# Kernel optimization log

Hardware: AMD Instinct MI355X
Metric: run time of the kernel (lower is better)

## Reference

```python
import jax, jax.numpy as jnp
import numpy as np

B, S, HID, QKV, H = 2, 4096, 1024, 1024, 16
HD = QKV // H  # head_dim = 64
KH, KW = 4, 1
SH, SW = 4, 1


def setup_inputs() -> dict:
    key = jax.random.key(0)
    ks = jax.random.split(key, 7)
    s = 1.0 / np.sqrt(HID)
    q = jax.random.normal(ks[0], (B, S, HID), dtype=jnp.float32)
    Wq = jax.random.uniform(ks[1], (HID, QKV), jnp.float32, -s, s)
    Wk = jax.random.uniform(ks[2], (HID, QKV), jnp.float32, -s, s)
    Wv = jax.random.uniform(ks[3], (HID, QKV), jnp.float32, -s, s)
    Wlin = jax.random.uniform(ks[4], (QKV, HID), jnp.float32, -1.0 / np.sqrt(QKV), 1.0 / np.sqrt(QKV))
    # depthwise conv weight: [out_ch=H, in_ch/groups=1, KH, KW]
    cs = 1.0 / np.sqrt(KH * KW)
    conv_w = jax.random.uniform(ks[5], (H, 1, KH, KW), jnp.float32, -cs, cs)
    log_temp = jnp.zeros((1,), dtype=jnp.float32)  # temperature='unit', frozen
    return {"q": q, "Wq": Wq, "Wk": Wk, "Wv": Wv, "Wlin": Wlin,
            "conv_w": conv_w, "log_temp": log_temp}


def split_heads(x):
    # [B, S, QKV] -> [B, H, S, HD]
    return x.reshape(B, -1, H, HD).transpose(0, 2, 1, 3)


def depthwise_conv(x, w):
    # x: [B, H, S, HD]; depthwise over channel dim H, window over (S, HD)
    return jax.lax.conv_general_dilated(
        x, w, window_strides=(SH, SW), padding='VALID',
        feature_group_count=H,
        dimension_numbers=('NCHW', 'OIHW', 'NCHW'))


def reference(q, Wq, Wk, Wv, Wlin, conv_w, log_temp):
    # self-attention path: k = v = q
    qh = split_heads(q @ Wq)          # [B,H,S,HD]
    kh = split_heads(q @ Wk)
    vh = split_heads(q @ Wv)
    qh = qh * (1.0 / jnp.exp(log_temp[0]))
    kc = depthwise_conv(kh, conv_w)   # [B,H,Sk,HD], Sk = (S-4)//4 + 1
    vc = depthwise_conv(vh, conv_w)
    logits_raw = jnp.einsum('bhqd,bhkd->bhqk', qh, kc)
    # shape changed after conv -> masks skipped (matches torch branch)
    att = jax.nn.softmax(logits_raw, axis=-1)
    out = jnp.einsum('bhqk,bhkd->bhqd', att, vc)  # [B,H,S,HD]
    out = out.transpose(0, 2, 1, 3).reshape(B, S, QKV)
    out = out @ Wlin                  # [B,S,HID]
    return (out, logits_raw)
```

## Files before the change

kernel.cpp:

```cpp
#include <hip/hip_runtime.h>
#include <hip/hip_bf16.h>
#include <stdint.h>


using short8 = __attribute__((ext_vector_type(8))) short;
using bf16x4 = __attribute__((ext_vector_type(4))) short;
using f32x4  = __attribute__((ext_vector_type(4))) float;

__device__ __forceinline__ float bf2f(short u) {
  union { float f; uint32_t i; } v; v.i = ((uint32_t)(uint16_t)u) << 16; return v.f;
}
__device__ __forceinline__ short f2bf(float f) {
  union { float f; uint32_t i; } v; v.f = f;
  uint32_t r = v.i + 0x7FFFu + ((v.i >> 16) & 1u);
  return (short)(uint16_t)(r >> 16);
}
__device__ __forceinline__ short f2bf_hw(float f) {
  __hip_bfloat16 h = __float2bfloat16(f);
  return *reinterpret_cast<short*>(&h);
}

__device__ __forceinline__ void async16(const void* g, void* l) {
  __builtin_amdgcn_global_load_lds(
      (const __attribute__((address_space(1))) void*)g,
      (__attribute__((address_space(3))) void*)l, 16, 0, 0);
}

__global__ void cvt8(const float* __restrict__ in, short* __restrict__ out) {
  const size_t i = ((size_t)blockIdx.x * 256 + threadIdx.x) * 8;
  float4 a = *(const float4*)(in + i);
  float4 b = *(const float4*)(in + i + 4);
  short8 o;
  o[0] = f2bf(a.x); o[1] = f2bf(a.y); o[2] = f2bf(a.z); o[3] = f2bf(a.w);
  o[4] = f2bf(b.x); o[5] = f2bf(b.y); o[6] = f2bf(b.z); o[7] = f2bf(b.w);
  *(short8*)(out + i) = o;
}

struct ConvT4Args { const float* s0; const float* s1; const float* s2;
                    const float* s3; short* out; };
__global__ void convT4(ConvT4Args a) {
  __shared__ float tile[64][65];
  const float* in = (blockIdx.z == 0) ? a.s0 : (blockIdx.z == 1) ? a.s1
                   : (blockIdx.z == 2) ? a.s2 : a.s3;
  short* out = a.out + (size_t)blockIdx.z * 1048576;
  const int c0 = blockIdx.x * 64, r0 = blockIdx.y * 64;
  const int tx = threadIdx.x & 63, ty = threadIdx.x >> 6;
  #pragma unroll
  for (int i = ty; i < 64; i += 4)
    tile[i][tx] = in[(size_t)(r0 + i) * 1024 + c0 + tx];
  __syncthreads();
  #pragma unroll
  for (int i = ty; i < 64; i += 4)
    out[(size_t)(c0 + i) * 1024 + r0 + tx] = f2bf(tile[tx][i]);
}

__global__ void transpose2d(const short* __restrict__ in, short* __restrict__ out,
                            int R, int C) {
  __shared__ short tile[64][65];
  const size_t zoff = (size_t)blockIdx.z * (size_t)R * (size_t)C;
  const int c0 = blockIdx.x * 64, r0 = blockIdx.y * 64;
  const int tx = threadIdx.x & 63, ty = threadIdx.x >> 6;
  #pragma unroll
  for (int i = ty; i < 64; i += 4)
    tile[i][tx] = in[zoff + (size_t)(r0 + i) * C + c0 + tx];
  __syncthreads();
  #pragma unroll
  for (int i = ty; i < 64; i += 4)
    out[zoff + (size_t)(c0 + i) * R + r0 + tx] = tile[tx][i];
}

struct GemmArgs {
  const short* A; const short* Bt;
  short* C; short* C2; short* C3; float* Cf;
  long sA, sB, sC;
  long zA, zB, zC;
  int  K;
  const float* ltemp;
  const float* cw;
  int  mode;
};

__global__ __launch_bounds__(256, 2)
void gemm_bt(GemmArgs g) {
  const int tid  = threadIdx.x;
  const int wave = tid >> 6, lane = tid & 63;
  const int l16 = lane & 15, l4 = lane >> 4;
  const int wm = wave & 1, wn = wave >> 1;
  const int m0 = blockIdx.y * 128, n0 = blockIdx.x * 128;
  const size_t zA = (size_t)blockIdx.z * g.zA;
  const size_t zB = (size_t)blockIdx.z * g.zB;
  const size_t zC = (size_t)blockIdx.z * g.zC;

  __shared__ __align__(16) short As[128 * 64];
  __shared__ __align__(16) short Bs[128 * 64];

  f32x4 acc[4][4] = {};

  const int srow = tid >> 3;
  const int scol = (tid & 7) << 3;
  const short* Abase = g.A + zA + (size_t)m0 * g.sA + scol;
  const short* Bbase = g.Bt + zB + (size_t)n0 * g.sB + scol;

  for (int k0 = 0; k0 < g.K; k0 += 64) {
    __syncthreads();
    #pragma unroll
    for (int c = 0; c < 4; ++c) {
      async16(Abase + (size_t)(c * 32 + srow) * g.sA + k0, &As[c * 2048 + wave * 512]);
      async16(Bbase + (size_t)(c * 32 + srow) * g.sB + k0, &Bs[c * 2048 + wave * 512]);
    }
    asm volatile("s_waitcnt vmcnt(0)" ::: "memory");
    __syncthreads();
    #pragma unroll
    for (int kk = 0; kk < 2; ++kk) {
      short8 a[4], b[4];
      #pragma unroll
      for (int t = 0; t < 4; ++t) {
        a[t] = *(const short8*)&As[(wm * 64 + t * 16 + l16) * 64 + kk * 32 + l4 * 8];
        b[t] = *(const short8*)&Bs[(wn * 64 + t * 16 + l16) * 64 + kk * 32 + l4 * 8];
      }
      #pragma unroll
      for (int i = 0; i < 4; ++i)
        #pragma unroll
        for (int j = 0; j < 4; ++j)
          acc[i][j] = __builtin_amdgcn_mfma_f32_16x16x32_bf16(a[i], b[j], acc[i][j], 0, 0, 0);
    }
  }

  if (g.mode == 0) {
    float* Cz = g.Cf + zC;
    #pragma unroll
    for (int i = 0; i < 4; ++i) {
      const int row = m0 + wm * 64 + i * 16 + l4 * 4;
      #pragma unroll
      for (int j = 0; j < 4; ++j) {
        const int col = n0 + wn * 64 + j * 16 + l16;
        #pragma unroll
        for (int rr = 0; rr < 4; ++rr)
          Cz[(size_t)(row + rr) * g.sC + col] = acc[i][j][rr];
      }
    }
  } else if (blockIdx.z == 0) {
    float sc = __expf(-g.ltemp[0]);
    short* Cz = g.C;
    #pragma unroll
    for (int i = 0; i < 4; ++i) {
      const int row = m0 + wm * 64 + i * 16 + l4 * 4;
      #pragma unroll
      for (int j = 0; j < 4; ++j) {
        const int col = n0 + wn * 64 + j * 16 + l16;
        const int hh = col >> 6, dd = col & 63;
        #pragma unroll
        for (int rr = 0; rr < 4; ++rr) {
          const int m = row + rr;
          const size_t off = (size_t)((m >> 12) * 16 + hh) * 262144
                           + (size_t)(m & 4095) * 64 + dd;
          Cz[off] = f2bf(acc[i][j][rr] * sc);
        }
      }
    }
  } else {
    const int h = (n0 + wn * 64) >> 6;
    float wv[4];
    #pragma unroll
    for (int t = 0; t < 4; ++t) wv[t] = g.cw[h * 4 + t];
    short* dst = (blockIdx.z == 1) ? g.C2 : g.C3;
    #pragma unroll
    for (int i = 0; i < 4; ++i) {
      const int row_base = m0 + wm * 64 + i * 16 + l4 * 4;
      const int b  = row_base >> 12;
      const int sk = (row_base & 4095) >> 2;
      #pragma unroll
      for (int j = 0; j < 4; ++j) {
        const int d = j * 16 + l16;
        float v = wv[0] * acc[i][j][0] + wv[1] * acc[i][j][1]
                + wv[2] * acc[i][j][2] + wv[3] * acc[i][j][3];
        dst[(size_t)(b * 16 + h) * 65536 + (size_t)sk * 64 + d] = f2bf(v);
      }
    }
  }
}

__global__ __launch_bounds__(256, 4)
void fused_attn(const short* __restrict__ qh, const short* __restrict__ kc,
                const short* __restrict__ vct,
                float* __restrict__ logits, short* __restrict__ oattn) {
  const int id = blockIdx.x;
  const int bh = id & 31;
  const int qt = id >> 5;
  const int tid = threadIdx.x;
  const int wave = tid >> 6, lane = tid & 63;
  const int l16 = lane & 15, l4 = lane >> 4;

  __shared__ __align__(16) short attb[4][32 * 128];
  short* const myatt = attb[wave];

  const int qg = qt * 128 + wave * 32;

  const short* qbase = qh + (size_t)bh * 262144 + (size_t)qg * 64;
  const short8 aQ0_0 = *(const short8*)(qbase + (size_t)l16 * 64 + l4 * 8);
  const short8 aQ0_1 = *(const short8*)(qbase + (size_t)l16 * 64 + 32 + l4 * 8);
  const short8 aQ1_0 = *(const short8*)(qbase + (size_t)(16 + l16) * 64 + l4 * 8);
  const short8 aQ1_1 = *(const short8*)(qbase + (size_t)(16 + l16) * 64 + 32 + l4 * 8);

  const short* kb = kc + (size_t)bh * 65536;
  const short* vb = vct + (size_t)bh * 65536;
  float* lgqA = logits + (size_t)bh * 4194304 + (size_t)(qg + l16) * 1024;
  float* lgqB = lgqA + 16 * 1024;

  const int sw = (l16 & 7) << 3;
  float psumA = 0.f, psumB = 0.f;
  f32x4 o0 = {}, o1 = {}, o2 = {}, o3 = {};
  f32x4 o4 = {}, o5 = {}, o6 = {}, o7 = {};

  for (int sec = 0; sec < 8; ++sec) {
    const int kbase = sec * 128;

    #pragma unroll 2
    for (int j = 0; j < 8; ++j) {
      const int kr = kbase + j * 16 + l16;
      short8 k0 = *(const short8*)(kb + (size_t)kr * 64 + l4 * 8);
      short8 k1 = *(const short8*)(kb + (size_t)kr * 64 + 32 + l4 * 8);
      f32x4 accA = {}, accB = {};
      accA = __builtin_amdgcn_mfma_f32_16x16x32_bf16(k0, aQ0_0, accA, 0, 0, 0);
      accA = __builtin_amdgcn_mfma_f32_16x16x32_bf16(k1, aQ0_1, accA, 0, 0, 0);
      accB = __builtin_amdgcn_mfma_f32_16x16x32_bf16(k0, aQ1_0, accB, 0, 0, 0);
      accB = __builtin_amdgcn_mfma_f32_16x16x32_bf16(k1, aQ1_1, accB, 0, 0, 0);

      *(f32x4*)(lgqA + kbase + j * 16 + l4 * 4) = accA;
      *(f32x4*)(lgqB + kbase + j * 16 + l4 * 4) = accB;

      bf16x4 pA, pB;
      #pragma unroll
      for (int rr = 0; rr < 4; ++rr) {
        const float eA = __expf(accA[rr]);
        const float eB = __expf(accB[rr]);
        psumA += eA;
        psumB += eB;
        pA[rr] = f2bf_hw(eA);
        pB[rr] = f2bf_hw(eB);
      }
      const int pc = (j * 16 + l4 * 4) ^ sw;
      *(bf16x4*)&myatt[l16 * 128 + pc] = pA;
      *(bf16x4*)&myatt[(16 + l16) * 128 + pc] = pB;
    }

    #pragma unroll
    for (int c = 0; c < 4; ++c) {
      const int cb = kbase + c * 32 + l4 * 8;
      const int cl = (c * 32 + l4 * 8) ^ sw;
      short8 paA = *(const short8*)&myatt[l16 * 128 + cl];
      short8 paB = *(const short8*)&myatt[(16 + l16) * 128 + cl];
      short8 v0 = *(const short8*)(vb + (size_t)(l16)      * 1024 + cb);
      short8 v1 = *(const short8*)(vb + (size_t)(16 + l16) * 1024 + cb);
      short8 v2 = *(const short8*)(vb + (size_t)(32 + l16) * 1024 + cb);
      short8 v3 = *(const short8*)(vb + (size_t)(48 + l16) * 1024 + cb);
      o0 = __builtin_amdgcn_mfma_f32_16x16x32_bf16(paA, v0, o0, 0, 0, 0);
      o1 = __builtin_amdgcn_mfma_f32_16x16x32_bf16(paA, v1, o1, 0, 0, 0);
      o2 = __builtin_amdgcn_mfma_f32_16x16x32_bf16(paA, v2, o2, 0, 0, 0);
      o3 = __builtin_amdgcn_mfma_f32_16x16x32_bf16(paA, v3, o3, 0, 0, 0);
      o4 = __builtin_amdgcn_mfma_f32_16x16x32_bf16(paB, v0, o4, 0, 0, 0);
      o5 = __builtin_amdgcn_mfma_f32_16x16x32_bf16(paB, v1, o5, 0, 0, 0);
      o6 = __builtin_amdgcn_mfma_f32_16x16x32_bf16(paB, v2, o6, 0, 0, 0);
      o7 = __builtin_amdgcn_mfma_f32_16x16x32_bf16(paB, v3, o7, 0, 0, 0);
    }
  }

  psumA += __shfl_xor(psumA, 16, 64);
  psumA += __shfl_xor(psumA, 32, 64);
  psumB += __shfl_xor(psumB, 16, 64);
  psumB += __shfl_xor(psumB, 32, 64);
  float invA[4], invB[4];
  #pragma unroll
  for (int rr = 0; rr < 4; ++rr) {
    invA[rr] = 1.0f / __shfl(psumA, l4 * 4 + rr, 64);
    invB[rr] = 1.0f / __shfl(psumB, l4 * 4 + rr, 64);
  }

  short* op = oattn + ((size_t)(bh >> 4) * 4096 + qg) * 1024 + (bh & 15) * 64;
  #pragma unroll
  for (int rr = 0; rr < 4; ++rr) {
    const size_t ra = (size_t)(l4 * 4 + rr) * 1024;
    op[ra + l16]      = f2bf(o0[rr] * invA[rr]);
    op[ra + 16 + l16] = f2bf(o1[rr] * invA[rr]);
    op[ra + 32 + l16] = f2bf(o2[rr] * invA[rr]);
    op[ra + 48 + l16] = f2bf(o3[rr] * invA[rr]);
    const size_t rb = (size_t)(16 + l4 * 4 + rr) * 1024;
    op[rb + l16]      = f2bf(o4[rr] * invB[rr]);
    op[rb + 16 + l16] = f2bf(o5[rr] * invB[rr]);
    op[rb + 32 + l16] = f2bf(o6[rr] * invB[rr]);
    op[rb + 48 + l16] = f2bf(o7[rr] * invB[rr]);
  }
}

extern "C" void kernel_launch(void* const* d_in, const int* in_sizes, int n_in,
                              void* d_out, int out_size, void* d_ws, size_t ws_size,
                              hipStream_t stream) {
  const float* q    = (const float*)d_in[0];
  const float* Wq   = (const float*)d_in[1];
  const float* Wk   = (const float*)d_in[2];
  const float* Wv   = (const float*)d_in[3];
  const float* Wlin = (const float*)d_in[4];
  const float* cw   = (const float*)d_in[5];
  const float* lt   = (const float*)d_in[6];

  float* out_f    = (float*)d_out;
  float* logits_f = out_f + 8388608;

  short* ws    = (short*)d_ws;
  short* Wt    = ws;
  short* Xb    = ws + 4194304;
  short* QKVq  = ws + 12582912;
  short* Kc    = ws + 20971520;
  short* Vc    = ws + 23068672;
  short* Vct   = ws + 25165824;
  short* oattn = Xb;

  cvt8<<<dim3(4096), 256, 0, stream>>>(q, Xb);

  ConvT4Args ca = { Wq, Wk, Wv, Wlin, Wt };
  convT4<<<dim3(16, 16, 4), 256, 0, stream>>>(ca);

  GemmArgs gq = {};
  gq.A = Xb; gq.Bt = Wt; gq.C = QKVq; gq.C2 = Kc; gq.C3 = Vc;
  gq.sA = 1024; gq.sB = 1024; gq.sC = 0;
  gq.zA = 0; gq.zB = 1048576; gq.zC = 0;
  gq.K = 1024; gq.ltemp = lt; gq.cw = cw; gq.mode = 3;
  gemm_bt<<<dim3(8, 64, 3), 256, 0, stream>>>(gq);

  transpose2d<<<dim3(1, 16, 32), 256, 0, stream>>>(Vc, Vct, 1024, 64);

  fused_attn<<<dim3(1024), 256, 0, stream>>>(QKVq, Kc, Vct, logits_f, oattn);

  GemmArgs gf = {};
  gf.A = oattn; gf.Bt = Wt + 3145728; gf.Cf = out_f;
  gf.sA = 1024; gf.sB = 1024; gf.sC = 1024;
  gf.zA = 0; gf.zB = 0; gf.zC = 0;
  gf.K = 1024; gf.mode = 0;
  gemm_bt<<<dim3(8, 64, 1), 256, 0, stream>>>(gf);
}
```

Measured before the change: 309.1 us.

## Stage K and V tiles in shared LDS with async double buffering

Each block now cooperatively loads 64-row K and V tiles into LDS with async global-to-LDS copies, double-buffered across 16 half-sections. The four waves then share those tiles instead of each issuing its own global loads for K and V. The per-wave probability buffer shrinks to match the smaller step. LDS use per block grows and the occupancy hint drops from 4 to 3 blocks. The change also adds a barrier per step and relies on a vmcnt wait count that must line up with the interleaved logits stores.

Measured after the change: 281.5 us. -8.9%, faster.

```diff
diff --git a/kernel.cpp b/kernel.cpp
--- a/kernel.cpp
+++ b/kernel.cpp
@@ -180,7 +180,7 @@
   }
 }
 
-__global__ __launch_bounds__(256, 4)
+__global__ __launch_bounds__(256, 3)
 void fused_attn(const short* __restrict__ qh, const short* __restrict__ kc,
                 const short* __restrict__ vct,
                 float* __restrict__ logits, short* __restrict__ oattn) {
@@ -191,7 +191,9 @@
   const int wave = tid >> 6, lane = tid & 63;
   const int l16 = lane & 15, l4 = lane >> 4;
 
-  __shared__ __align__(16) short attb[4][32 * 128];
+  __shared__ __align__(16) short Ks[2][4096];
+  __shared__ __align__(16) short Vs[2][4096];
+  __shared__ __align__(16) short attb[4][2048];
   short* const myatt = attb[wave];
 
   const int qg = qt * 128 + wave * 32;
@@ -207,19 +209,46 @@
   float* lgqA = logits + (size_t)bh * 4194304 + (size_t)(qg + l16) * 1024;
   float* lgqB = lgqA + 16 * 1024;
 
+  const int strow = tid >> 3;
+  const int schunk = (tid & 7) ^ (strow & 7);
+  const int sdst = tid * 8;
+
   const int sw = (l16 & 7) << 3;
   float psumA = 0.f, psumB = 0.f;
   f32x4 o0 = {}, o1 = {}, o2 = {}, o3 = {};
   f32x4 o4 = {}, o5 = {}, o6 = {}, o7 = {};
 
-  for (int sec = 0; sec < 8; ++sec) {
-    const int kbase = sec * 128;
-
-    #pragma unroll 2
-    for (int j = 0; j < 8; ++j) {
-      const int kr = kbase + j * 16 + l16;
-      short8 k0 = *(const short8*)(kb + (size_t)kr * 64 + l4 * 8);
-      short8 k1 = *(const short8*)(kb + (size_t)kr * 64 + 32 + l4 * 8);
+  short* ksc = Ks[0]; short* ksn = Ks[1];
+  short* vsc = Vs[0]; short* vsn = Vs[1];
+
+  #pragma unroll
+  for (int ri = 0; ri < 2; ++ri) {
+    const int row = ri * 32 + strow;
+    async16(kb + (size_t)row * 64 + schunk * 8, ksc + ri * 2048 + sdst);
+    async16(vb + (size_t)row * 1024 + schunk * 8, vsc + ri * 2048 + sdst);
+  }
+  asm volatile("s_waitcnt vmcnt(0)" ::: "memory");
+  __syncthreads();
+
+  for (int hs = 0; hs < 16; ++hs) {
+    const int kbase = hs * 64;
+
+    if (hs < 15) {
+      #pragma unroll
+      for (int ri = 0; ri < 2; ++ri) {
+        const int row = ri * 32 + strow;
+        async16(kb + (size_t)(kbase + 64 + row) * 64 + schunk * 8,
+                ksn + ri * 2048 + sdst);
+        async16(vb + (size_t)row * 1024 + (kbase + 64) + schunk * 8,
+                vsn + ri * 2048 + sdst);
+      }
+    }
+
+    #pragma unroll
+    for (int j = 0; j < 4; ++j) {
+      const int row = j * 16 + l16;
+      short8 k0 = *(const short8*)&ksc[row * 64 + ((l4 ^ (l16 & 7)) << 3)];
+      short8 k1 = *(const short8*)&ksc[row * 64 + (((4 + l4) ^ (l16 & 7)) << 3)];
       f32x4 accA = {}, accB = {};
       accA = __builtin_amdgcn_mfma_f32_16x16x32_bf16(k0, aQ0_0, accA, 0, 0, 0);
       accA = __builtin_amdgcn_mfma_f32_16x16x32_bf16(k1, aQ0_1, accA, 0, 0, 0);
@@ -240,20 +269,20 @@
         pB[rr] = f2bf_hw(eB);
       }
       const int pc = (j * 16 + l4 * 4) ^ sw;
-      *(bf16x4*)&myatt[l16 * 128 + pc] = pA;
-      *(bf16x4*)&myatt[(16 + l16) * 128 + pc] = pB;
-    }
-
-    #pragma unroll
-    for (int c = 0; c < 4; ++c) {
-      const int cb = kbase + c * 32 + l4 * 8;
+      *(bf16x4*)&myatt[l16 * 64 + pc] = pA;
+      *(bf16x4*)&myatt[(16 + l16) * 64 + pc] = pB;
+    }
+
+    #pragma unroll
+    for (int c = 0; c < 2; ++c) {
       const int cl = (c * 32 + l4 * 8) ^ sw;
-      short8 paA = *(const short8*)&myatt[l16 * 128 + cl];
-      short8 paB = *(const short8*)&myatt[(16 + l16) * 128 + cl];
-      short8 v0 = *(const short8*)(vb + (size_t)(l16)      * 1024 + cb);
-      short8 v1 = *(const short8*)(vb + (size_t)(16 + l16) * 1024 + cb);
-      short8 v2 = *(const short8*)(vb + (size_t)(32 + l16) * 1024 + cb);
-      short8 v3 = *(const short8*)(vb + (size_t)(48 + l16) * 1024 + cb);
+      const int vch = ((c * 4 + l4) ^ (l16 & 7)) << 3;
+      short8 paA = *(const short8*)&myatt[l16 * 64 + cl];
+      short8 paB = *(const short8*)&myatt[(16 + l16) * 64 + cl];
+      short8 v0 = *(const short8*)&vsc[(l16) * 64 + vch];
+      short8 v1 = *(const short8*)&vsc[(16 + l16) * 64 + vch];
+      short8 v2 = *(const short8*)&vsc[(32 + l16) * 64 + vch];
+      short8 v3 = *(const short8*)&vsc[(48 + l16) * 64 + vch];
       o0 = __builtin_amdgcn_mfma_f32_16x16x32_bf16(paA, v0, o0, 0, 0, 0);
       o1 = __builtin_amdgcn_mfma_f32_16x16x32_bf16(paA, v1, o1, 0, 0, 0);
       o2 = __builtin_amdgcn_mfma_f32_16x16x32_bf16(paA, v2, o2, 0, 0, 0);
@@ -262,6 +291,14 @@
       o5 = __builtin_amdgcn_mfma_f32_16x16x32_bf16(paB, v1, o5, 0, 0, 0);
       o6 = __builtin_amdgcn_mfma_f32_16x16x32_bf16(paB, v2, o6, 0, 0, 0);
       o7 = __builtin_amdgcn_mfma_f32_16x16x32_bf16(paB, v3, o7, 0, 0, 0);
+    }
+
+    if (hs < 15) {
+      asm volatile("s_waitcnt vmcnt(8)" ::: "memory");
+      __syncthreads();
+      short* t;
+      t = ksc; ksc = ksn; ksn = t;
+      t = vsc; vsc = vsn; vsn = t;
     }
   }
 
```
